# Kernel optimization log

Measured on AMD Instinct MI355X. Metric: run time of the kernel, lower is better.

## Reference

```python
import jax, jax.numpy as jnp
import numpy as np

B, H, W, C = 4, 64, 64, 256
CQ = C // 8


def setup_inputs() -> dict:
    key = jax.random.key(0)
    ks = jax.random.split(key, 5)
    scale = 0.02
    inputs = jax.random.normal(ks[0], (B, H, W, C), dtype=jnp.float32)
    wq = jax.random.normal(ks[1], (C, CQ), dtype=jnp.float32) * scale
    bq = jnp.zeros((CQ,), dtype=jnp.float32)
    wk = jax.random.normal(ks[2], (C, CQ), dtype=jnp.float32) * scale
    bk = jnp.zeros((CQ,), dtype=jnp.float32)
    wv = jax.random.normal(ks[3], (C, C), dtype=jnp.float32) * scale
    bv = jnp.zeros((C,), dtype=jnp.float32)
    gamma = jax.random.normal(ks[4], (), dtype=jnp.float32)
    return {"inputs": inputs, "wq": wq, "bq": bq, "wk": wk, "bk": bk,
            "wv": wv, "bv": bv, "gamma": gamma}


def reference(inputs, wq, bq, wk, bk, wv, bv, gamma):
    b, h, w, c = inputs.shape
    n = h * w
    x = inputs.reshape(b, n, c)  # [B, N, C]
    # 1x1 convs == per-pixel linear projections
    q = x @ wq + bq              # [B, N, Cq]
    k = x @ wk + bk              # [B, N, Cq]
    v = x @ wv + bv              # [B, N, C]
    # energy = Q K^T (no sqrt scaling, as in the original)
    energy = jnp.einsum('bnd,bmd->bnm', q, k)      # [B, N, N]
    attention = jax.nn.softmax(energy, axis=-1)    # softmax over keys
    # x_out = V^T @ attention^T -> per query: sum_m attn[n,m] * v[m]
    x_out = jnp.einsum('bnm,bmc->bnc', attention, v)  # [B, N, C]
    x_out = x_out.reshape(b, h, w, c)
    return gamma * x_out + inputs
```

## Files before the change

kernel.cpp:

```cpp
#include <hip/hip_runtime.h>
#include <hip/hip_bf16.h>

typedef __attribute__((ext_vector_type(8))) short bf16x8;
typedef __attribute__((ext_vector_type(4))) float f32x4;
typedef __attribute__((ext_vector_type(16))) float f32x16;
typedef __attribute__((ext_vector_type(4))) int int4v;

#define NB 4
#define NN 4096
#define NC 256
#define NSPLIT 4
#define KEYS_PER_SPLIT 1024
#define KT_ITERS 16
#define LOG2E 1.4426950408889634f

__device__ __forceinline__ unsigned short f2bf(float f) {
    unsigned u = __builtin_bit_cast(unsigned, f);
    u += 0x7fffu + ((u >> 16) & 1u);
    return (unsigned short)(u >> 16);
}
__device__ __forceinline__ float bf2f(unsigned short u) {
    unsigned v = ((unsigned)u) << 16;
    return __builtin_bit_cast(float, v);
}
__device__ __forceinline__ void load_lds16(const void* g, void* l) {
    __builtin_amdgcn_global_load_lds(
        (const __attribute__((address_space(1))) void*)g,
        (__attribute__((address_space(3))) void*)l, 16, 0, 0);
}
__device__ __forceinline__ unsigned cvtpk(float lo, float hi) {
    unsigned d;
    asm("v_cvt_pk_bf16_f32 %0, %1, %2" : "=v"(d) : "v"(lo), "v"(hi));
    return d;
}
__device__ __forceinline__ void pl32swap(unsigned &a, unsigned &b) {
    asm volatile("v_permlane32_swap_b32 %0, %1" : "+v"(a), "+v"(b));
}
__device__ __forceinline__ float fexp2(float x) {
    float r;
    asm("v_exp_f32 %0, %1" : "=v"(r) : "v"(x));
    return r;
}

__global__ __launch_bounds__(256) void wt_kernel(
    const float* __restrict__ wq, const float* __restrict__ wk,
    const float* __restrict__ wv, unsigned short* __restrict__ wt)
{
    const int c = blockIdx.x;
    const int k = threadIdx.x;
    float v;
    if (c < 32)      v = wq[k * 32 + c];
    else if (c < 64) v = wk[k * 32 + (c - 32)] * LOG2E;
    else             v = wv[k * 256 + (c - 64)];
    wt[c * 256 + k] = f2bf(v);
}

__global__ __launch_bounds__(256) void proj_kernel(
    const float* __restrict__ x,
    const unsigned short* __restrict__ wt,
    const float* __restrict__ bq, const float* __restrict__ bk,
    const float* __restrict__ bv,
    unsigned short* __restrict__ q_ws,
    unsigned short* __restrict__ k_ws,
    unsigned short* __restrict__ vt_ws)
{
    const int lane = threadIdx.x & 63;
    const int w    = threadIdx.x >> 6;
    const int l15  = lane & 15, hh = lane >> 4;
    const int m0   = blockIdx.x * 16;
    const int ct0  = w * 5;

    f32x4 acc[5];
    #pragma unroll
    for (int i = 0; i < 5; ++i) acc[i] = f32x4{0.f, 0.f, 0.f, 0.f};

    const float* xrow = x + (size_t)(m0 + l15) * 256 + hh * 8;
    #pragma unroll
    for (int ks = 0; ks < 8; ++ks) {
        float4 xa = ((const float4*)(xrow + ks * 32))[0];
        float4 xb = ((const float4*)(xrow + ks * 32))[1];
        bf16x8 afrag;
        afrag[0] = (short)f2bf(xa.x); afrag[1] = (short)f2bf(xa.y);
        afrag[2] = (short)f2bf(xa.z); afrag[3] = (short)f2bf(xa.w);
        afrag[4] = (short)f2bf(xb.x); afrag[5] = (short)f2bf(xb.y);
        afrag[6] = (short)f2bf(xb.z); afrag[7] = (short)f2bf(xb.w);
        #pragma unroll
        for (int c = 0; c < 5; ++c) {
            bf16x8 bfrag = *(const bf16x8*)(wt + (size_t)((ct0 + c) * 16 + l15) * 256 + ks * 32 + hh * 8);
            acc[c] = __builtin_amdgcn_mfma_f32_16x16x32_bf16(afrag, bfrag, acc[c], 0, 0, 0);
        }
    }

    const int b    = m0 >> 12;
    const int nloc = m0 & 4095;
    #pragma unroll
    for (int c = 0; c < 5; ++c) {
        const int ct = ct0 + c;
        const int c0 = ct * 16;
        float bias;
        if (c0 < 32)      bias = bq[c0 + l15];
        else if (c0 < 64) bias = bk[c0 - 32 + l15] * LOG2E;
        else              bias = bv[c0 - 64 + l15];
        if (c0 < 64) {
            unsigned short* dst = (c0 < 32) ? q_ws : k_ws;
            const int cc = (c0 < 32) ? c0 : (c0 - 32);
            #pragma unroll
            for (int i = 0; i < 4; ++i)
                dst[(size_t)(m0 + hh * 4 + i) * 32 + cc + l15] = f2bf(acc[c][i] + bias);
        } else {
            const int cc = c0 - 64 + l15;
            #pragma unroll
            for (int i = 0; i < 4; i += 2) {
                unsigned lo = f2bf(acc[c][i]     + bias);
                unsigned hi = f2bf(acc[c][i + 1] + bias);
                *(unsigned*)(vt_ws + ((size_t)b * 256 + cc) * 4096 + nloc + hh * 4 + i)
                    = lo | (hi << 16);
            }
        }
    }
}

__global__ __launch_bounds__(512, 4) void attn_kernel(
    const unsigned short* __restrict__ q_ws,
    const unsigned short* __restrict__ k_ws,
    const unsigned short* __restrict__ vt_ws,
    unsigned short* __restrict__ opart,
    float* __restrict__ lpart)
{
    __shared__ unsigned short vt_lds[2 * 256 * 64];

    const int lane = threadIdx.x & 63;
    const int wid  = threadIdx.x >> 6;
    const int l31  = lane & 31;
    const int hi   = lane >> 5;
    const int wr   = wid >> 1;
    const int wc   = wid & 1;

    const int xcd   = blockIdx.x & 7;
    const int j     = blockIdx.x >> 3;
    const int combo = xcd * 2 + (j >> 5);
    const int qtile = j & 31;
    const int split = combo >> 2;
    const int b     = combo & 3;
    const int q0    = qtile * 128;
    const int key0  = split * KEYS_PER_SPLIT;

    bf16x8 aq[2];
    #pragma unroll
    for (int cs = 0; cs < 2; ++cs)
        aq[cs] = *(const bf16x8*)(q_ws +
            (size_t)(b * 4096 + q0 + wr * 32 + l31) * 32 + cs * 16 + hi * 8);

    f32x16 acc[4];
    #pragma unroll
    for (int ct = 0; ct < 4; ++ct)
        #pragma unroll
        for (int r = 0; r < 16; ++r) acc[ct][r] = 0.f;
    float lsum = 0.f;

    const unsigned short* vt_base = vt_ws + (size_t)b * 256 * 4096;
    const unsigned short* k_base  = k_ws + (size_t)b * 4096 * 32;

    #pragma unroll
    for (int e = 0; e < 4; ++e) {
        int idx  = e * 512 + threadIdx.x;
        int c    = idx >> 3;
        int slot = idx & 7;
        const unsigned short* src = vt_base + (size_t)c * 4096 + key0 + ((slot ^ (c & 7)) << 3);
        load_lds16(src, (char*)vt_lds + idx * 16);
    }

    for (int kt = 0; kt < KT_ITERS; ++kt) {
        const int kb      = key0 + kt * 64;
        const int cur_off = (kt & 1) << 15;

        __syncthreads();

        if (kt + 1 < KT_ITERS) {
            const int nxt_off = cur_off ^ 32768;
            #pragma unroll
            for (int e = 0; e < 4; ++e) {
                int idx  = e * 512 + threadIdx.x;
                int c    = idx >> 3;
                int slot = idx & 7;
                const unsigned short* src = vt_base + (size_t)c * 4096 + (kb + 64) + ((slot ^ (c & 7)) << 3);
                load_lds16(src, (char*)vt_lds + nxt_off + idx * 16);
            }
        }

        unsigned pa[4][4];
        #pragma unroll
        for (int ktile = 0; ktile < 2; ++ktile) {
            bf16x8 ak0 = *(const bf16x8*)(k_base +
                (size_t)(kb + ktile * 32 + l31) * 32 + hi * 8);
            bf16x8 ak1 = *(const bf16x8*)(k_base +
                (size_t)(kb + ktile * 32 + l31) * 32 + 16 + hi * 8);
            f32x16 e0;
            #pragma unroll
            for (int r = 0; r < 16; ++r) e0[r] = 0.f;
            e0 = __builtin_amdgcn_mfma_f32_32x32x16_bf16(ak0, aq[0], e0, 0, 0, 0);
            e0 = __builtin_amdgcn_mfma_f32_32x32x16_bf16(ak1, aq[1], e0, 0, 0, 0);

            float s = 0.f;
            #pragma unroll
            for (int h = 0; h < 2; ++h) {
                float p0 = fexp2(e0[h*8+0]), p1 = fexp2(e0[h*8+1]);
                float p2 = fexp2(e0[h*8+2]), p3 = fexp2(e0[h*8+3]);
                float p4 = fexp2(e0[h*8+4]), p5 = fexp2(e0[h*8+5]);
                float p6 = fexp2(e0[h*8+6]), p7 = fexp2(e0[h*8+7]);
                s += ((p0 + p1) + (p2 + p3)) + ((p4 + p5) + (p6 + p7));
                unsigned d0 = cvtpk(p0, p1);
                unsigned d1 = cvtpk(p2, p3);
                unsigned d2 = cvtpk(p4, p5);
                unsigned d3 = cvtpk(p6, p7);
                pl32swap(d0, d2);
                pl32swap(d1, d3);
                const int ks = ktile * 2 + h;
                pa[ks][0] = d0; pa[ks][1] = d1;
                pa[ks][2] = d2; pa[ks][3] = d3;
            }
            lsum += s;
        }

        __builtin_amdgcn_s_setprio(1);
        #pragma unroll
        for (int ks = 0; ks < 4; ++ks) {
            union { unsigned u[4]; bf16x8 v; } cvt;
            cvt.u[0] = pa[ks][0]; cvt.u[1] = pa[ks][1];
            cvt.u[2] = pa[ks][2]; cvt.u[3] = pa[ks][3];
            #pragma unroll
            for (int ct = 0; ct < 4; ++ct) {
                int c = wc * 128 + ct * 32 + l31;
                int chunk = ks * 2 + hi;
                bf16x8 bvf = *(const bf16x8*)((char*)vt_lds + cur_off + c * 128 + ((chunk ^ (c & 7)) << 4));
                acc[ct] = __builtin_amdgcn_mfma_f32_32x32x16_bf16(cvt.v, bvf, acc[ct], 0, 0, 0);
            }
        }
        __builtin_amdgcn_s_setprio(0);
    }

    lsum += __shfl_xor(lsum, 32);

    const size_t rowb = (size_t)(split * 4 + b) * 4096 + q0 + wr * 32;
    if (wc == 0 && hi == 0)
        lpart[rowb + l31] = lsum;

    #pragma unroll
    for (int ct = 0; ct < 4; ++ct) {
        int col = wc * 128 + ct * 32 + l31;
        #pragma unroll
        for (int rr = 0; rr < 16; ++rr) {
            int row = (rr & 3) + 8 * (rr >> 2) + 4 * hi;
            opart[(rowb + row) * 256 + col] = f2bf(acc[ct][rr]);
        }
    }
}

__global__ __launch_bounds__(256) void combine_kernel(
    const unsigned short* __restrict__ opart,
    const float* __restrict__ lpart,
    const float* __restrict__ x,
    const float* __restrict__ gamma_p,
    float* __restrict__ out)
{
    const int t  = blockIdx.x * 256 + threadIdx.x;
    const int r  = t >> 5;
    const int c0 = (t & 31) * 8;
    const float gamma = gamma_p[0];

    float sumO[8];
    #pragma unroll
    for (int j = 0; j < 8; ++j) sumO[j] = 0.f;
    float suml = 0.f;
    #pragma unroll
    for (int s = 0; s < NSPLIT; ++s) {
        bf16x8 o = *(const bf16x8*)(opart + ((size_t)(s * 16384 + r)) * 256 + c0);
        #pragma unroll
        for (int j = 0; j < 8; ++j) sumO[j] += bf2f((unsigned short)o[j]);
        suml += lpart[s * 16384 + r];
    }
    const float inv = gamma / suml;
    const size_t base = (size_t)r * 256 + c0;
    float4 x0 = *(const float4*)(x + base);
    float4 x1 = *(const float4*)(x + base + 4);
    float4 o0, o1;
    o0.x = sumO[0] * inv + x0.x; o0.y = sumO[1] * inv + x0.y;
    o0.z = sumO[2] * inv + x0.z; o0.w = sumO[3] * inv + x0.w;
    o1.x = sumO[4] * inv + x1.x; o1.y = sumO[5] * inv + x1.y;
    o1.z = sumO[6] * inv + x1.z; o1.w = sumO[7] * inv + x1.w;
    *(float4*)(out + base)     = o0;
    *(float4*)(out + base + 4) = o1;
}

extern "C" void kernel_launch(void* const* d_in, const int* in_sizes, int n_in,
                              void* d_out, int out_size, void* d_ws, size_t ws_size,
                              hipStream_t stream) {
    const float* x     = (const float*)d_in[0];
    const float* wq    = (const float*)d_in[1];
    const float* bq    = (const float*)d_in[2];
    const float* wk    = (const float*)d_in[3];
    const float* bk    = (const float*)d_in[4];
    const float* wv    = (const float*)d_in[5];
    const float* bv    = (const float*)d_in[6];
    const float* gamma = (const float*)d_in[7];
    float* out = (float*)d_out;

    char* ws = (char*)d_ws;
    unsigned short* wt    = (unsigned short*)(ws);
    unsigned short* q_ws  = (unsigned short*)(ws + 163840);
    unsigned short* k_ws  = (unsigned short*)(ws + 1212416);
    unsigned short* vt_ws = (unsigned short*)(ws + 2260992);
    unsigned short* opart = (unsigned short*)(ws + 10649600);
    float*          lpart = (float*)(ws + 44204032);

    wt_kernel     <<<320,  256, 0, stream>>>(wq, wk, wv, wt);
    proj_kernel   <<<1024, 256, 0, stream>>>(x, wt, bq, bk, bv, q_ws, k_ws, vt_ws);
    attn_kernel   <<<512,  512, 0, stream>>>(q_ws, k_ws, vt_ws, opart, lpart);
    combine_kernel<<<2048, 256, 0, stream>>>(opart, lpart, x, gamma, out);
}
```

Before: 103.3 us.

## Stage K tiles through LDS double buffer and unroll key loop by two

K fragments are now prefetched into a double-buffered LDS region with async global-to-LDS loads, alongside the V tiles, instead of being read from global memory right before the QK MFMAs. The key loop is manually unrolled by two through a macro so that buffer offsets become compile-time constants. The aim is to hide K load latency behind the previous iteration's compute and to remove per-iteration offset arithmetic. It costs a little extra LDS and relies on the existing barrier to order the K buffer reuse.

```diff
diff --git a/kernel.cpp b/kernel.cpp
--- a/kernel.cpp
+++ b/kernel.cpp
@@ -120,6 +120,77 @@
     }
 }
 
+#define ATTN_BODY(KB, CUR_V, CUR_K, NXT_V, NXT_K, PREFETCH)                         \
+    {                                                                               \
+        __syncthreads();                                                            \
+        if (PREFETCH) {                                                             \
+            _Pragma("unroll")                                                       \
+            for (int e = 0; e < 4; ++e) {                                           \
+                int idx  = e * 512 + threadIdx.x;                                   \
+                int c    = idx >> 3;                                                \
+                int slot = idx & 7;                                                 \
+                const unsigned short* src = vt_base + (size_t)c * 4096 +            \
+                    ((KB) + 64) + ((slot ^ (c & 7)) << 3);                          \
+                load_lds16(src, (char*)vt_lds + (NXT_V) + idx * 16);                \
+            }                                                                       \
+            if (wid < 4) {                                                          \
+                const unsigned short* ksrc = k_base +                               \
+                    (size_t)(((KB) + 64) + (wid >> 1) * 32 + l31) * 32 +            \
+                    (wid & 1) * 16 + hi * 8;                                        \
+                load_lds16(ksrc, (char*)k_lds + (NXT_K) + wid * 1024 + lane * 16);  \
+            }                                                                       \
+        }                                                                           \
+        unsigned pa[4][4];                                                          \
+        _Pragma("unroll")                                                           \
+        for (int ktile = 0; ktile < 2; ++ktile) {                                   \
+            bf16x8 ak0 = *(const bf16x8*)((char*)k_lds + (CUR_K) +                  \
+                                          (ktile * 2 + 0) * 1024 + lane * 16);      \
+            bf16x8 ak1 = *(const bf16x8*)((char*)k_lds + (CUR_K) +                  \
+                                          (ktile * 2 + 1) * 1024 + lane * 16);      \
+            f32x16 e0;                                                              \
+            _Pragma("unroll")                                                       \
+            for (int r = 0; r < 16; ++r) e0[r] = 0.f;                               \
+            e0 = __builtin_amdgcn_mfma_f32_32x32x16_bf16(ak0, aq[0], e0, 0, 0, 0);  \
+            e0 = __builtin_amdgcn_mfma_f32_32x32x16_bf16(ak1, aq[1], e0, 0, 0, 0);  \
+            float s = 0.f;                                                          \
+            _Pragma("unroll")                                                       \
+            for (int h = 0; h < 2; ++h) {                                           \
+                float p0 = fexp2(e0[h*8+0]), p1 = fexp2(e0[h*8+1]);                 \
+                float p2 = fexp2(e0[h*8+2]), p3 = fexp2(e0[h*8+3]);                 \
+                float p4 = fexp2(e0[h*8+4]), p5 = fexp2(e0[h*8+5]);                 \
+                float p6 = fexp2(e0[h*8+6]), p7 = fexp2(e0[h*8+7]);                 \
+                s += ((p0 + p1) + (p2 + p3)) + ((p4 + p5) + (p6 + p7));             \
+                unsigned d0 = cvtpk(p0, p1);                                        \
+                unsigned d1 = cvtpk(p2, p3);                                        \
+                unsigned d2 = cvtpk(p4, p5);                                        \
+                unsigned d3 = cvtpk(p6, p7);                                        \
+                pl32swap(d0, d2);                                                   \
+                pl32swap(d1, d3);                                                   \
+                const int ks = ktile * 2 + h;                                       \
+                pa[ks][0] = d0; pa[ks][1] = d1;                                     \
+                pa[ks][2] = d2; pa[ks][3] = d3;                                     \
+            }                                                                       \
+            lsum += s;                                                              \
+        }                                                                           \
+        __builtin_amdgcn_s_setprio(1);                                              \
+        _Pragma("unroll")                                                           \
+        for (int ks = 0; ks < 4; ++ks) {                                            \
+            union { unsigned u[4]; bf16x8 v; } cvt;                                 \
+            cvt.u[0] = pa[ks][0]; cvt.u[1] = pa[ks][1];                             \
+            cvt.u[2] = pa[ks][2]; cvt.u[3] = pa[ks][3];                             \
+            _Pragma("unroll")                                                       \
+            for (int ct = 0; ct < 4; ++ct) {                                        \
+                int c = wc * 128 + ct * 32 + l31;                                   \
+                int chunk = ks * 2 + hi;                                            \
+                bf16x8 bvf = *(const bf16x8*)((char*)vt_lds + (CUR_V) +             \
+                    c * 128 + ((chunk ^ (c & 7)) << 4));                            \
+                acc[ct] = __builtin_amdgcn_mfma_f32_32x32x16_bf16(cvt.v, bvf,       \
+                                                                  acc[ct], 0, 0, 0);\
+            }                                                                       \
+        }                                                                           \
+        __builtin_amdgcn_s_setprio(0);                                              \
+    }
+
 __global__ __launch_bounds__(512, 4) void attn_kernel(
     const unsigned short* __restrict__ q_ws,
     const unsigned short* __restrict__ k_ws,
@@ -128,6 +199,7 @@
     float* __restrict__ lpart)
 {
     __shared__ unsigned short vt_lds[2 * 256 * 64];
+    __shared__ unsigned short k_lds[2 * 2048];
 
     const int lane = threadIdx.x & 63;
     const int wid  = threadIdx.x >> 6;
@@ -169,74 +241,16 @@
         const unsigned short* src = vt_base + (size_t)c * 4096 + key0 + ((slot ^ (c & 7)) << 3);
         load_lds16(src, (char*)vt_lds + idx * 16);
     }
-
-    for (int kt = 0; kt < KT_ITERS; ++kt) {
-        const int kb      = key0 + kt * 64;
-        const int cur_off = (kt & 1) << 15;
-
-        __syncthreads();
-
-        if (kt + 1 < KT_ITERS) {
-            const int nxt_off = cur_off ^ 32768;
-            #pragma unroll
-            for (int e = 0; e < 4; ++e) {
-                int idx  = e * 512 + threadIdx.x;
-                int c    = idx >> 3;
-                int slot = idx & 7;
-                const unsigned short* src = vt_base + (size_t)c * 4096 + (kb + 64) + ((slot ^ (c & 7)) << 3);
-                load_lds16(src, (char*)vt_lds + nxt_off + idx * 16);
-            }
-        }
-
-        unsigned pa[4][4];
-        #pragma unroll
-        for (int ktile = 0; ktile < 2; ++ktile) {
-            bf16x8 ak0 = *(const bf16x8*)(k_base +
-                (size_t)(kb + ktile * 32 + l31) * 32 + hi * 8);
-            bf16x8 ak1 = *(const bf16x8*)(k_base +
-                (size_t)(kb + ktile * 32 + l31) * 32 + 16 + hi * 8);
-            f32x16 e0;
-            #pragma unroll
-            for (int r = 0; r < 16; ++r) e0[r] = 0.f;
-            e0 = __builtin_amdgcn_mfma_f32_32x32x16_bf16(ak0, aq[0], e0, 0, 0, 0);
-            e0 = __builtin_amdgcn_mfma_f32_32x32x16_bf16(ak1, aq[1], e0, 0, 0, 0);
-
-            float s = 0.f;
-            #pragma unroll
-            for (int h = 0; h < 2; ++h) {
-                float p0 = fexp2(e0[h*8+0]), p1 = fexp2(e0[h*8+1]);
-                float p2 = fexp2(e0[h*8+2]), p3 = fexp2(e0[h*8+3]);
-                float p4 = fexp2(e0[h*8+4]), p5 = fexp2(e0[h*8+5]);
-                float p6 = fexp2(e0[h*8+6]), p7 = fexp2(e0[h*8+7]);
-                s += ((p0 + p1) + (p2 + p3)) + ((p4 + p5) + (p6 + p7));
-                unsigned d0 = cvtpk(p0, p1);
-                unsigned d1 = cvtpk(p2, p3);
-                unsigned d2 = cvtpk(p4, p5);
-                unsigned d3 = cvtpk(p6, p7);
-                pl32swap(d0, d2);
-                pl32swap(d1, d3);
-                const int ks = ktile * 2 + h;
-                pa[ks][0] = d0; pa[ks][1] = d1;
-                pa[ks][2] = d2; pa[ks][3] = d3;
-            }
-            lsum += s;
-        }
-
-        __builtin_amdgcn_s_setprio(1);
-        #pragma unroll
-        for (int ks = 0; ks < 4; ++ks) {
-            union { unsigned u[4]; bf16x8 v; } cvt;
-            cvt.u[0] = pa[ks][0]; cvt.u[1] = pa[ks][1];
-            cvt.u[2] = pa[ks][2]; cvt.u[3] = pa[ks][3];
-            #pragma unroll
-            for (int ct = 0; ct < 4; ++ct) {
-                int c = wc * 128 + ct * 32 + l31;
-                int chunk = ks * 2 + hi;
-                bf16x8 bvf = *(const bf16x8*)((char*)vt_lds + cur_off + c * 128 + ((chunk ^ (c & 7)) << 4));
-                acc[ct] = __builtin_amdgcn_mfma_f32_32x32x16_bf16(cvt.v, bvf, acc[ct], 0, 0, 0);
-            }
-        }
-        __builtin_amdgcn_s_setprio(0);
+    if (wid < 4) {
+        const unsigned short* ksrc = k_base +
+            (size_t)(key0 + (wid >> 1) * 32 + l31) * 32 + (wid & 1) * 16 + hi * 8;
+        load_lds16(ksrc, (char*)k_lds + wid * 1024 + lane * 16);
+    }
+
+    for (int kt2 = 0; kt2 < 8; ++kt2) {
+        const int kb = key0 + kt2 * 128;
+        ATTN_BODY(kb,      0,     0,    32768, 4096, true)
+        ATTN_BODY(kb + 64, 32768, 4096, 0,     0,    (kt2 != 7))
     }
 
     lsum += __shfl_xor(lsum, 32);
```

Measured after the change: 148.2 us. 43.4% more time.
